# Performance work log

Measured on AMD Instinct MI355X. Metric: run time of the kernel, lower is better.

Reference implementation:

```python
import jax, jax.numpy as jnp
import numpy as np

C_IN, C_OUT, K, DG, PAD = 256, 256, 3, 2, 1
EPS = 1e-5


def setup_inputs() -> dict:
    key = jax.random.key(0)
    k = jax.random.split(key, 8)
    B, H, W = 4, 64, 64
    x = jax.random.normal(k[0], (B, C_IN, H, W), jnp.float32)
    # offset/mask conv (DCNv2 pack): 3 * dg * k * k output channels
    w_off = jax.random.normal(k[1], (3 * DG * K * K, C_IN, K, K), jnp.float32) * 0.01
    b_off = jnp.zeros((3 * DG * K * K,), jnp.float32)
    # main deformable conv weight
    w = jax.random.normal(k[2], (C_OUT, C_IN, K, K), jnp.float32) * (1.0 / np.sqrt(C_IN * K * K))
    b = jnp.zeros((C_OUT,), jnp.float32)
    # BatchNorm (eval mode: running stats)
    gamma = jnp.ones((C_OUT,), jnp.float32)
    beta = jnp.zeros((C_OUT,), jnp.float32)
    running_mean = jax.random.normal(k[3], (C_OUT,), jnp.float32) * 0.1
    running_var = jax.random.uniform(k[4], (C_OUT,), jnp.float32, 0.5, 1.5)
    return dict(x=x, w_off=w_off, b_off=b_off, w=w, b=b, gamma=gamma, beta=beta,
                running_mean=running_mean, running_var=running_var)


def _conv2d_same(x, w, b):
    y = jax.lax.conv_general_dilated(x, w, (1, 1), 'SAME',
                                     dimension_numbers=('NCHW', 'OIHW', 'NCHW'))
    return y + b[None, :, None, None]


def _deform_conv(x, w_off, b_off, w, b):
    B, C, H, W = x.shape
    K2 = K * K
    Cg = C // DG
    # offsets + modulation mask from internal conv (DCNv2 pack)
    om = _conv2d_same(x, w_off, b_off)            # [B, 3*DG*K2, H, W]
    o1, o2, m = jnp.split(om, 3, axis=1)
    mask = jax.nn.sigmoid(m).reshape(B, DG, 1, K2, H * W)
    off_y = o1.reshape(B, DG, K2, H, W)
    off_x = o2.reshape(B, DG, K2, H, W)
    # base sampling grid: output pixel + kernel tap - pad
    ki = jnp.arange(K)
    ky = (jnp.repeat(ki, K) - PAD).astype(jnp.float32)   # [K2]
    kx = (jnp.tile(ki, K) - PAD).astype(jnp.float32)     # [K2]
    py = off_y + ky[:, None, None] + jnp.arange(H, dtype=jnp.float32)[None, :, None]
    px = off_x + kx[:, None, None] + jnp.arange(W, dtype=jnp.float32)[None, None, :]
    y0 = jnp.floor(py)
    x0 = jnp.floor(px)
    ly = (py - y0).reshape(B, DG, 1, K2, H * W)
    lx = (px - x0).reshape(B, DG, 1, K2, H * W)
    y0i = y0.astype(jnp.int32)
    x0i = x0.astype(jnp.int32)
    xg = x.reshape(B, DG, Cg, H * W)

    def gather(yi, xi):
        # zero-padded bilinear corner gather, per deformable group
        valid = (yi >= 0) & (yi < H) & (xi >= 0) & (xi < W)
        lin = jnp.clip(yi, 0, H - 1) * W + jnp.clip(xi, 0, W - 1)
        v = jnp.take_along_axis(xg[:, :, :, None, :],
                                lin.reshape(B, DG, 1, K2, H * W), axis=-1)
        return v * valid.reshape(B, DG, 1, K2, H * W)

    val = (gather(y0i, x0i) * (1 - ly) * (1 - lx)
           + gather(y0i, x0i + 1) * (1 - ly) * lx
           + gather(y0i + 1, x0i) * ly * (1 - lx)
           + gather(y0i + 1, x0i + 1) * ly * lx)
    val = val * mask                               # [B, DG, Cg, K2, H*W]
    wr = w.reshape(C_OUT, DG, Cg, K2)
    out = jnp.einsum('bgckn,ogck->bon', val, wr).reshape(B, C_OUT, H, W)
    return out + b[None, :, None, None]


def reference(x, w_off, b_off, w, b, gamma, beta, running_mean, running_var):
    y = _deform_conv(x, w_off, b_off, w, b)
    inv = gamma / jnp.sqrt(running_var + EPS)
    y = (y - running_mean[None, :, None, None]) * inv[None, :, None, None] + beta[None, :, None, None]
    return jax.nn.relu(y)
```

## Files before the change

### kernel.cpp

```cpp
#include <hip/hip_runtime.h>
#include <math.h>

typedef __bf16 bf16x8 __attribute__((ext_vector_type(8)));
typedef float  f32x4  __attribute__((ext_vector_type(4)));
typedef int    i32x4  __attribute__((ext_vector_type(4)));

#define MFMA16(a, b, c) __builtin_amdgcn_mfma_f32_16x16x32_bf16((a), (b), (c), 0, 0, 0)

#define ATIDX(r, c) ((r) * 128 + (((c) ^ ((r) & 7)) * 8))

__global__ __launch_bounds__(256) void setup_kernel(
    const float* __restrict__ x, const float* __restrict__ w,
    const float* __restrict__ w_off, const float* __restrict__ bconv,
    const float* __restrict__ gamma, const float* __restrict__ beta,
    const float* __restrict__ mean, const float* __restrict__ var,
    __bf16* __restrict__ xT, __bf16* __restrict__ wFragD,
    __bf16* __restrict__ wFragO, float* __restrict__ sc,
    float* __restrict__ sh) {
  int t = threadIdx.x;
  if (blockIdx.x < 1024) {
    __shared__ float xs[64][65];
    int b = blockIdx.x >> 8, y = (blockIdx.x >> 2) & 63, cc = blockIdx.x & 3;
    for (int i = t; i < 4096; i += 256) {
      int cl = i >> 6, xc = i & 63;
      xs[cl][xc] = x[(((size_t)b * 256 + cc * 64 + cl) * 64 + y) * 64 + xc];
    }
    __syncthreads();
    for (int i = t; i < 4096; i += 256) {
      int xc = i >> 6, cl = i & 63;
      xT[(((size_t)b * 64 + y) * 64 + xc) * 256 + cc * 64 + cl] = (__bf16)xs[cl][xc];
    }
    return;
  }
  int i = (blockIdx.x - 1024) * 256 + t;
  if (i < 589824) {
    int j = i & 7, lane = (i >> 3) & 63, ocb = (i >> 9) & 15;
    int kc = (i >> 13) & 3, gk = i >> 15;
    int klocal = (lane >> 4) * 8 + j;
    int oc = ocb * 16 + (lane & 15);
    int c = kc * 32 + klocal;
    int g = gk / 9, ktap = gk % 9;
    wFragD[i] = (__bf16)w[((size_t)oc * 256 + g * 128 + c) * 9 + ktap];
  } else {
    int i2 = i - 589824;
    int j = i2 & 7, lane = (i2 >> 3) & 63, ocb = (i2 >> 9) & 3;
    int kc = (i2 >> 11) & 7, tap = i2 >> 14;
    int klocal = (lane >> 4) * 8 + j;
    int oc = ocb * 16 + (lane & 15);
    int ci = kc * 32 + klocal;
    wFragO[i2] = (oc < 54) ? (__bf16)w_off[((size_t)oc * 256 + ci) * 9 + tap]
                           : (__bf16)0.f;
  }
  if (i < 256) {
    float s = gamma[i] * rsqrtf(var[i] + 1e-5f);
    sc[i] = s;
    sh[i] = (bconv[i] - mean[i]) * s + beta[i];
  }
}

struct PhaseC {
  f32x4 swgtv[18 * 64];
  i32x4 slinv[18 * 64];
  __bf16 atile[2][64 * 128];
};
union FusedLDS {
  __bf16 rowbuf[3 * 66 * 256];
  PhaseC c;
};

__global__ __launch_bounds__(512) void fused_kernel(
    const __bf16* __restrict__ xT, const __bf16* __restrict__ wFragD,
    const __bf16* __restrict__ wFragO, const float* __restrict__ b_off,
    const float* __restrict__ sc, const float* __restrict__ sh,
    float* __restrict__ out) {
  __shared__ __attribute__((aligned(16))) FusedLDS U;
  __shared__ float omrow[54 * 64];
  int t = threadIdx.x;
  int b = blockIdx.x >> 6, y = blockIdx.x & 63;
  int lane = t & 63, wv = t >> 6;
  int l15 = lane & 15, quad = lane >> 4;
  const __bf16* xTb = xT + (size_t)b * 64 * 64 * 256;
  bf16x8 z8;
  #pragma unroll
  for (int e = 0; e < 8; ++e) z8[e] = (__bf16)0.f;

  for (int i = t; i < 3 * 66 * 32; i += 512) {
    int c = i & 31, px66 = (i >> 5) % 66, dy = i / 2112;
    int y2 = y + dy - 1, x2 = px66 - 1;
    bf16x8 v = z8;
    if (y2 >= 0 && y2 < 64 && x2 >= 0 && x2 < 64)
      v = *(const bf16x8*)(xTb + ((size_t)y2 * 64 + x2) * 256 + c * 8);
    *(bf16x8*)&U.rowbuf[dy * 16896 + px66 * 256 + ((c ^ (px66 & 7)) * 8)] = v;
  }
  __syncthreads();

  {
    int mh = wv & 1, ocq = wv >> 1;
    f32x4 acc0 = {0.f, 0.f, 0.f, 0.f};
    f32x4 acc1 = {0.f, 0.f, 0.f, 0.f};
    for (int tap = 0; tap < 9; ++tap) {
      int dy = tap / 3, dxs = tap % 3;
      const __bf16* bb = wFragO + ((size_t)(tap * 8) * 4 + ocq) * 512 + lane * 8;
      bf16x8 Bf[8];
      #pragma unroll
      for (int kc = 0; kc < 8; ++kc)
        Bf[kc] = *(const bf16x8*)(bb + (size_t)kc * 4 * 512);
      int p0 = mh * 32 + l15 + dxs, p1 = p0 + 16;
      const __bf16* rb = U.rowbuf + dy * 16896;
      #pragma unroll
      for (int kc = 0; kc < 8; ++kc) {
        int c = kc * 4 + quad;
        bf16x8 a0 = *(const bf16x8*)&rb[p0 * 256 + ((c ^ (p0 & 7)) * 8)];
        bf16x8 a1 = *(const bf16x8*)&rb[p1 * 256 + ((c ^ (p1 & 7)) * 8)];
        acc0 = MFMA16(a0, Bf[kc], acc0);
        acc1 = MFMA16(a1, Bf[kc], acc1);
      }
    }
    int oc = ocq * 16 + l15;
    if (oc < 54) {
      float bo = b_off[oc];
      #pragma unroll
      for (int fm = 0; fm < 2; ++fm) {
        f32x4 v = fm ? acc1 : acc0;
        f32x4 r = {v.x + bo, v.y + bo, v.z + bo, v.w + bo};
        int pxs = mh * 32 + fm * 16 + quad * 4;
        *(f32x4*)&omrow[oc * 64 + pxs] = r;
      }
    }
  }
  __syncthreads();

  for (int i = t; i < 18 * 64; i += 512) {
    int gk = i >> 6, p = i & 63;
    int k = gk % 9;
    float oy = omrow[gk * 64 + p];
    float ox = omrow[(18 + gk) * 64 + p];
    float mz = omrow[(36 + gk) * 64 + p];
    float mv = 1.f / (1.f + expf(-mz));
    float py  = (float)(y + (k / 3) - 1) + oy;
    float pxf = (float)(p + (k % 3) - 1) + ox;
    float y0f = floorf(py), x0f = floorf(pxf);
    int y0 = (int)y0f, x0 = (int)x0f;
    float ly = py - y0f, lx = pxf - x0f;
    int y1 = y0 + 1, x1 = x0 + 1;
    bool vy0 = (y0 >= 0) && (y0 < 64), vy1 = (y1 >= 0) && (y1 < 64);
    bool vx0 = (x0 >= 0) && (x0 < 64), vx1 = (x1 >= 0) && (x1 < 64);
    int cy0 = min(max(y0, 0), 63), cy1 = min(max(y1, 0), 63);
    int cx0 = min(max(x0, 0), 63), cx1 = min(max(x1, 0), 63);
    f32x4 sv;
    sv.x = (vy0 && vx0) ? (1.f - ly) * (1.f - lx) * mv : 0.f;
    sv.y = (vy0 && vx1) ? (1.f - ly) * lx * mv : 0.f;
    sv.z = (vy1 && vx0) ? ly * (1.f - lx) * mv : 0.f;
    sv.w = (vy1 && vx1) ? ly * lx * mv : 0.f;
    i32x4 lv;
    lv.x = (cy0 * 64 + cx0) * 256;
    lv.y = (cy0 * 64 + cx1) * 256;
    lv.z = (cy1 * 64 + cx0) * 256;
    lv.w = (cy1 * 64 + cx1) * 256;
    U.c.swgtv[i] = sv;
    U.c.slinv[i] = lv;
  }

  f32x4 acc[4][2];
  #pragma unroll
  for (int fm = 0; fm < 4; ++fm)
    #pragma unroll
    for (int fn = 0; fn < 2; ++fn)
      acc[fm][fn] = (f32x4){0.f, 0.f, 0.f, 0.f};

  __syncthreads();

  int ch0 = l15 * 8;
  {
    const __bf16* xg = xTb + ch0;
    #pragma unroll
    for (int j = 0; j < 2; ++j) {
      int p = wv * 8 + j * 4 + quad;
      f32x4 sv = U.c.swgtv[p];
      i32x4 lv = U.c.slinv[p];
      bf16x8 c0 = *(const bf16x8*)(xg + lv.x);
      bf16x8 c1 = *(const bf16x8*)(xg + lv.y);
      bf16x8 c2 = *(const bf16x8*)(xg + lv.z);
      bf16x8 c3 = *(const bf16x8*)(xg + lv.w);
      bf16x8 o;
      #pragma unroll
      for (int e = 0; e < 8; ++e)
        o[e] = (__bf16)(sv.x * (float)c0[e] + sv.y * (float)c1[e]
                      + sv.z * (float)c2[e] + sv.w * (float)c3[e]);
      *(bf16x8*)&U.c.atile[0][ATIDX(p, l15)] = o;
    }
  }
  bf16x8 Bf[8];
  {
    const __bf16* bb = wFragD + ((size_t)wv * 2) * 512 + lane * 8;
    #pragma unroll
    for (int kc = 0; kc < 4; ++kc) {
      Bf[kc * 2]     = *(const bf16x8*)(bb + (size_t)kc * 16 * 512);
      Bf[kc * 2 + 1] = *(const bf16x8*)(bb + (size_t)kc * 16 * 512 + 512);
    }
  }

  for (int gk = 0; gk < 18; ++gk) {
    __syncthreads();
    bf16x8 cr[2][4];
    f32x4 sv[2];
    int pj[2];
    if (gk < 17) {
      int gn = gk + 1;
      const __bf16* xg = xTb + (gn / 9) * 128 + ch0;
      #pragma unroll
      for (int j = 0; j < 2; ++j) {
        int p = wv * 8 + j * 4 + quad;
        pj[j] = p;
        sv[j] = U.c.swgtv[gn * 64 + p];
        i32x4 lv = U.c.slinv[gn * 64 + p];
        cr[j][0] = *(const bf16x8*)(xg + lv.x);
        cr[j][1] = *(const bf16x8*)(xg + lv.y);
        cr[j][2] = *(const bf16x8*)(xg + lv.z);
        cr[j][3] = *(const bf16x8*)(xg + lv.w);
      }
    }
    const __bf16* at = U.c.atile[gk & 1];
    #pragma unroll
    for (int kc = 0; kc < 4; ++kc) {
      #pragma unroll
      for (int fm = 0; fm < 4; ++fm) {
        bf16x8 a = *(const bf16x8*)&at[ATIDX(fm * 16 + l15, kc * 4 + quad)];
        acc[fm][0] = MFMA16(a, Bf[kc * 2],     acc[fm][0]);
        acc[fm][1] = MFMA16(a, Bf[kc * 2 + 1], acc[fm][1]);
      }
    }
    if (gk < 17) {
      __bf16* dst = U.c.atile[(gk + 1) & 1];
      #pragma unroll
      for (int j = 0; j < 2; ++j) {
        bf16x8 o;
        #pragma unroll
        for (int e = 0; e < 8; ++e)
          o[e] = (__bf16)(sv[j].x * (float)cr[j][0][e] + sv[j].y * (float)cr[j][1][e]
                        + sv[j].z * (float)cr[j][2][e] + sv[j].w * (float)cr[j][3][e]);
        *(bf16x8*)&dst[ATIDX(pj[j], l15)] = o;
      }
      const __bf16* bb = wFragD + ((size_t)((gk + 1) * 4) * 16 + wv * 2) * 512 + lane * 8;
      #pragma unroll
      for (int kc = 0; kc < 4; ++kc) {
        Bf[kc * 2]     = *(const bf16x8*)(bb + (size_t)kc * 16 * 512);
        Bf[kc * 2 + 1] = *(const bf16x8*)(bb + (size_t)kc * 16 * 512 + 512);
      }
    }
  }

  #pragma unroll
  for (int fm = 0; fm < 4; ++fm) {
    #pragma unroll
    for (int fn = 0; fn < 2; ++fn) {
      int oc = wv * 32 + fn * 16 + l15;
      float s = sc[oc], h = sh[oc];
      f32x4 v = acc[fm][fn];
      f32x4 r = {fmaxf(v.x * s + h, 0.f), fmaxf(v.y * s + h, 0.f),
                 fmaxf(v.z * s + h, 0.f), fmaxf(v.w * s + h, 0.f)};
      int pxs = fm * 16 + quad * 4;
      *(f32x4*)(out + (((size_t)b * 256 + oc) * 64 + y) * 64 + pxs) = r;
    }
  }
}

extern "C" void kernel_launch(void* const* d_in, const int* in_sizes, int n_in,
                              void* d_out, int out_size, void* d_ws, size_t ws_size,
                              hipStream_t stream) {
  const float* x     = (const float*)d_in[0];
  const float* w_off = (const float*)d_in[1];
  const float* b_off = (const float*)d_in[2];
  const float* w     = (const float*)d_in[3];
  const float* bconv = (const float*)d_in[4];
  const float* gamma = (const float*)d_in[5];
  const float* beta  = (const float*)d_in[6];
  const float* rmean = (const float*)d_in[7];
  const float* rvar  = (const float*)d_in[8];
  float* out = (float*)d_out;

  __bf16* xT     = (__bf16*)d_ws;
  __bf16* wFragD = (__bf16*)((char*)d_ws + 8388608);
  __bf16* wFragO = (__bf16*)((char*)d_ws + 9568256);
  float*  sc     = (float*)((char*)d_ws + 9863168);
  float*  sh     = (float*)((char*)d_ws + 9864192);

  setup_kernel<<<1024 + 2880, 256, 0, stream>>>(
      x, w, w_off, bconv, gamma, beta, rmean, rvar, xT, wFragD, wFragO, sc, sh);
  fused_kernel<<<4 * 64, 512, 0, stream>>>(xT, wFragD, wFragO, b_off, sc, sh, out);
}
```

Measured before the change: 131.5 us.

## Warp-specialize deformable conv into gather and MFMA waves, coalesce weight repack

The fused kernel now runs 1024 threads per block. Eight waves do the bilinear gather for the next tap group while the other eight run the MFMA GEMM on the current tile, replacing the old scheme where every wave did both in turn. The offset conv is split across 16 waves with one M tile each, and B fragments are streamed per k-chunk instead of held as eight registers. The setup kernel repacks the weights through shared memory in per-block tiles so global reads are coalesced, cutting the block count. The risk is that only half the waves issue MFMAs, and the larger block may hurt register allocation and occupancy.

```diff
diff --git a/kernel.cpp b/kernel.cpp
--- a/kernel.cpp
+++ b/kernel.cpp
@@ -17,44 +17,63 @@
     __bf16* __restrict__ xT, __bf16* __restrict__ wFragD,
     __bf16* __restrict__ wFragO, float* __restrict__ sc,
     float* __restrict__ sh) {
+  __shared__ float ws[16 * 128 * 9];
   int t = threadIdx.x;
   if (blockIdx.x < 1024) {
-    __shared__ float xs[64][65];
     int b = blockIdx.x >> 8, y = (blockIdx.x >> 2) & 63, cc = blockIdx.x & 3;
     for (int i = t; i < 4096; i += 256) {
       int cl = i >> 6, xc = i & 63;
-      xs[cl][xc] = x[(((size_t)b * 256 + cc * 64 + cl) * 64 + y) * 64 + xc];
+      ws[cl * 65 + xc] = x[(((size_t)b * 256 + cc * 64 + cl) * 64 + y) * 64 + xc];
     }
     __syncthreads();
     for (int i = t; i < 4096; i += 256) {
       int xc = i >> 6, cl = i & 63;
-      xT[(((size_t)b * 64 + y) * 64 + xc) * 256 + cc * 64 + cl] = (__bf16)xs[cl][xc];
+      xT[(((size_t)b * 64 + y) * 64 + xc) * 256 + cc * 64 + cl] =
+          (__bf16)ws[cl * 65 + xc];
     }
     return;
   }
-  int i = (blockIdx.x - 1024) * 256 + t;
-  if (i < 589824) {
-    int j = i & 7, lane = (i >> 3) & 63, ocb = (i >> 9) & 15;
-    int kc = (i >> 13) & 3, gk = i >> 15;
-    int klocal = (lane >> 4) * 8 + j;
-    int oc = ocb * 16 + (lane & 15);
-    int c = kc * 32 + klocal;
-    int g = gk / 9, ktap = gk % 9;
-    wFragD[i] = (__bf16)w[((size_t)oc * 256 + g * 128 + c) * 9 + ktap];
-  } else {
-    int i2 = i - 589824;
-    int j = i2 & 7, lane = (i2 >> 3) & 63, ocb = (i2 >> 9) & 3;
-    int kc = (i2 >> 11) & 7, tap = i2 >> 14;
-    int klocal = (lane >> 4) * 8 + j;
-    int oc = ocb * 16 + (lane & 15);
-    int ci = kc * 32 + klocal;
-    wFragO[i2] = (oc < 54) ? (__bf16)w_off[((size_t)oc * 256 + ci) * 9 + tap]
-                           : (__bf16)0.f;
-  }
-  if (i < 256) {
-    float s = gamma[i] * rsqrtf(var[i] + 1e-5f);
-    sc[i] = s;
-    sh[i] = (bconv[i] - mean[i]) * s + beta[i];
+  if (blockIdx.x < 1056) {
+    int id = blockIdx.x - 1024;
+    int g = id >> 4, ocb = id & 15;
+    for (int i = t; i < 18432; i += 256) {
+      int oc_l = i / 1152, rem = i % 1152;
+      ws[oc_l * 1152 + rem] = w[(size_t)(ocb * 16 + oc_l) * 2304 + g * 1152 + rem];
+    }
+    __syncthreads();
+    for (int i = t; i < 18432; i += 256) {
+      int j = i & 7, lane8 = (i >> 3) & 63, kc = (i >> 9) & 3, ktap = i >> 11;
+      int klocal = (lane8 >> 4) * 8 + j;
+      int oc_l = lane8 & 15, ci_l = kc * 32 + klocal;
+      float v = ws[oc_l * 1152 + ci_l * 9 + ktap];
+      int gk = g * 9 + ktap;
+      wFragD[((size_t)(gk * 4 + kc) * 16 + ocb) * 512 + (i & 511)] = (__bf16)v;
+    }
+    return;
+  }
+  {
+    int id2 = blockIdx.x - 1056;
+    int ocb = id2 >> 1, h = id2 & 1;
+    for (int i = t; i < 18432; i += 256) {
+      int oc_l = i / 1152, rem = i % 1152;
+      int oc = ocb * 16 + oc_l;
+      ws[oc_l * 1152 + rem] =
+          (oc < 54) ? w_off[(size_t)oc * 2304 + h * 1152 + rem] : 0.f;
+    }
+    __syncthreads();
+    for (int i = t; i < 18432; i += 256) {
+      int j = i & 7, lane8 = (i >> 3) & 63, kcl = (i >> 9) & 3, ktap = i >> 11;
+      int klocal = (lane8 >> 4) * 8 + j;
+      int oc_l = lane8 & 15, ci_l = kcl * 32 + klocal;
+      int kc = h * 4 + kcl;
+      float v = ws[oc_l * 1152 + ci_l * 9 + ktap];
+      wFragO[((size_t)(ktap * 8 + kc) * 4 + ocb) * 512 + (i & 511)] = (__bf16)v;
+    }
+    if (id2 == 0 && t < 256) {
+      float s = gamma[t] * rsqrtf(var[t] + 1e-5f);
+      sc[t] = s;
+      sh[t] = (bconv[t] - mean[t]) * s + beta[t];
+    }
   }
 }
 
@@ -68,7 +87,7 @@
   PhaseC c;
 };
 
-__global__ __launch_bounds__(512) void fused_kernel(
+__global__ __launch_bounds__(1024) void fused_kernel(
     const __bf16* __restrict__ xT, const __bf16* __restrict__ wFragD,
     const __bf16* __restrict__ wFragO, const float* __restrict__ b_off,
     const float* __restrict__ sc, const float* __restrict__ sh,
@@ -84,7 +103,7 @@
   #pragma unroll
   for (int e = 0; e < 8; ++e) z8[e] = (__bf16)0.f;
 
-  for (int i = t; i < 3 * 66 * 32; i += 512) {
+  for (int i = t; i < 3 * 66 * 32; i += 1024) {
     int c = i & 31, px66 = (i >> 5) % 66, dy = i / 2112;
     int y2 = y + dy - 1, x2 = px66 - 1;
     bf16x8 v = z8;
@@ -95,9 +114,8 @@
   __syncthreads();
 
   {
-    int mh = wv & 1, ocq = wv >> 1;
+    int mq = wv & 3, ocq = wv >> 2;
     f32x4 acc0 = {0.f, 0.f, 0.f, 0.f};
-    f32x4 acc1 = {0.f, 0.f, 0.f, 0.f};
     for (int tap = 0; tap < 9; ++tap) {
       int dy = tap / 3, dxs = tap % 3;
       const __bf16* bb = wFragO + ((size_t)(tap * 8) * 4 + ocq) * 512 + lane * 8;
@@ -105,32 +123,25 @@
       #pragma unroll
       for (int kc = 0; kc < 8; ++kc)
         Bf[kc] = *(const bf16x8*)(bb + (size_t)kc * 4 * 512);
-      int p0 = mh * 32 + l15 + dxs, p1 = p0 + 16;
+      int p0 = mq * 16 + l15 + dxs;
       const __bf16* rb = U.rowbuf + dy * 16896;
       #pragma unroll
       for (int kc = 0; kc < 8; ++kc) {
         int c = kc * 4 + quad;
         bf16x8 a0 = *(const bf16x8*)&rb[p0 * 256 + ((c ^ (p0 & 7)) * 8)];
-        bf16x8 a1 = *(const bf16x8*)&rb[p1 * 256 + ((c ^ (p1 & 7)) * 8)];
         acc0 = MFMA16(a0, Bf[kc], acc0);
-        acc1 = MFMA16(a1, Bf[kc], acc1);
       }
     }
     int oc = ocq * 16 + l15;
     if (oc < 54) {
       float bo = b_off[oc];
-      #pragma unroll
-      for (int fm = 0; fm < 2; ++fm) {
-        f32x4 v = fm ? acc1 : acc0;
-        f32x4 r = {v.x + bo, v.y + bo, v.z + bo, v.w + bo};
-        int pxs = mh * 32 + fm * 16 + quad * 4;
-        *(f32x4*)&omrow[oc * 64 + pxs] = r;
-      }
-    }
-  }
-  __syncthreads();
-
-  for (int i = t; i < 18 * 64; i += 512) {
+      f32x4 r = {acc0.x + bo, acc0.y + bo, acc0.z + bo, acc0.w + bo};
+      *(f32x4*)&omrow[oc * 64 + mq * 16 + quad * 4] = r;
+    }
+  }
+  __syncthreads();
+
+  for (int i = t; i < 18 * 64; i += 1024) {
     int gk = i >> 6, p = i & 63;
     int k = gk % 9;
     float oy = omrow[gk * 64 + p];
@@ -160,107 +171,99 @@
     U.c.swgtv[i] = sv;
     U.c.slinv[i] = lv;
   }
+  __syncthreads();
+
+  {
+    int p = t >> 4, c16 = t & 15;
+    const __bf16* xg = xTb + c16 * 8;
+    f32x4 sv = U.c.swgtv[p];
+    i32x4 lv = U.c.slinv[p];
+    bf16x8 c0 = *(const bf16x8*)(xg + lv.x);
+    bf16x8 c1 = *(const bf16x8*)(xg + lv.y);
+    bf16x8 c2 = *(const bf16x8*)(xg + lv.z);
+    bf16x8 c3 = *(const bf16x8*)(xg + lv.w);
+    bf16x8 o;
+    #pragma unroll
+    for (int e = 0; e < 8; ++e)
+      o[e] = (__bf16)(sv.x * (float)c0[e] + sv.y * (float)c1[e]
+                    + sv.z * (float)c2[e] + sv.w * (float)c3[e]);
+    *(bf16x8*)&U.c.atile[0][ATIDX(p, c16)] = o;
+  }
 
   f32x4 acc[4][2];
   #pragma unroll
-  for (int fm = 0; fm < 4; ++fm)
+  for (int fm = 0; fm < 4; ++fm) {
+    acc[fm][0] = (f32x4){0.f, 0.f, 0.f, 0.f};
+    acc[fm][1] = (f32x4){0.f, 0.f, 0.f, 0.f};
+  }
+  int nq = wv - 8;
+  bf16x8 bn0, bn1;
+  if (wv >= 8) {
+    const __bf16* bb = wFragD + ((size_t)nq * 2) * 512 + lane * 8;
+    bn0 = *(const bf16x8*)bb;
+    bn1 = *(const bf16x8*)(bb + 512);
+  }
+  __syncthreads();
+
+  for (int gk = 0; gk < 18; ++gk) {
+    if (wv < 8) {
+      if (gk < 17) {
+        int gn = gk + 1;
+        int c16 = t & 15, p = t >> 4;
+        const __bf16* xg = xTb + (gn / 9) * 128 + c16 * 8;
+        __bf16* dst = U.c.atile[(gk + 1) & 1];
+        #pragma unroll
+        for (int half = 0; half < 2; ++half) {
+          int pp = p + half * 32;
+          f32x4 sv = U.c.swgtv[gn * 64 + pp];
+          i32x4 lv = U.c.slinv[gn * 64 + pp];
+          bf16x8 c0 = *(const bf16x8*)(xg + lv.x);
+          bf16x8 c1 = *(const bf16x8*)(xg + lv.y);
+          bf16x8 c2 = *(const bf16x8*)(xg + lv.z);
+          bf16x8 c3 = *(const bf16x8*)(xg + lv.w);
+          bf16x8 o;
+          #pragma unroll
+          for (int e = 0; e < 8; ++e)
+            o[e] = (__bf16)(sv.x * (float)c0[e] + sv.y * (float)c1[e]
+                          + sv.z * (float)c2[e] + sv.w * (float)c3[e]);
+          *(bf16x8*)&dst[ATIDX(pp, c16)] = o;
+        }
+      }
+    } else {
+      const __bf16* at = U.c.atile[gk & 1];
+      #pragma unroll
+      for (int kc = 0; kc < 4; ++kc) {
+        bf16x8 b0 = bn0, b1 = bn1;
+        int nidx = gk * 4 + kc + 1;
+        if (nidx < 72) {
+          const __bf16* bb = wFragD + ((size_t)nidx * 16 + nq * 2) * 512 + lane * 8;
+          bn0 = *(const bf16x8*)bb;
+          bn1 = *(const bf16x8*)(bb + 512);
+        }
+        #pragma unroll
+        for (int fm = 0; fm < 4; ++fm) {
+          bf16x8 a = *(const bf16x8*)&at[ATIDX(fm * 16 + l15, kc * 4 + quad)];
+          acc[fm][0] = MFMA16(a, b0, acc[fm][0]);
+          acc[fm][1] = MFMA16(a, b1, acc[fm][1]);
+        }
+      }
+    }
+    __syncthreads();
+  }
+
+  if (wv >= 8) {
     #pragma unroll
-    for (int fn = 0; fn < 2; ++fn)
-      acc[fm][fn] = (f32x4){0.f, 0.f, 0.f, 0.f};
-
-  __syncthreads();
-
-  int ch0 = l15 * 8;
-  {
-    const __bf16* xg = xTb + ch0;
-    #pragma unroll
-    for (int j = 0; j < 2; ++j) {
-      int p = wv * 8 + j * 4 + quad;
-      f32x4 sv = U.c.swgtv[p];
-      i32x4 lv = U.c.slinv[p];
-      bf16x8 c0 = *(const bf16x8*)(xg + lv.x);
-      bf16x8 c1 = *(const bf16x8*)(xg + lv.y);
-      bf16x8 c2 = *(const bf16x8*)(xg + lv.z);
-      bf16x8 c3 = *(const bf16x8*)(xg + lv.w);
-      bf16x8 o;
-      #pragma unroll
-      for (int e = 0; e < 8; ++e)
-        o[e] = (__bf16)(sv.x * (float)c0[e] + sv.y * (float)c1[e]
-                      + sv.z * (float)c2[e] + sv.w * (float)c3[e]);
-      *(bf16x8*)&U.c.atile[0][ATIDX(p, l15)] = o;
-    }
-  }
-  bf16x8 Bf[8];
-  {
-    const __bf16* bb = wFragD + ((size_t)wv * 2) * 512 + lane * 8;
-    #pragma unroll
-    for (int kc = 0; kc < 4; ++kc) {
-      Bf[kc * 2]     = *(const bf16x8*)(bb + (size_t)kc * 16 * 512);
-      Bf[kc * 2 + 1] = *(const bf16x8*)(bb + (size_t)kc * 16 * 512 + 512);
-    }
-  }
-
-  for (int gk = 0; gk < 18; ++gk) {
-    __syncthreads();
-    bf16x8 cr[2][4];
-    f32x4 sv[2];
-    int pj[2];
-    if (gk < 17) {
-      int gn = gk + 1;
-      const __bf16* xg = xTb + (gn / 9) * 128 + ch0;
-      #pragma unroll
-      for (int j = 0; j < 2; ++j) {
-        int p = wv * 8 + j * 4 + quad;
-        pj[j] = p;
-        sv[j] = U.c.swgtv[gn * 64 + p];
-        i32x4 lv = U.c.slinv[gn * 64 + p];
-        cr[j][0] = *(const bf16x8*)(xg + lv.x);
-        cr[j][1] = *(const bf16x8*)(xg + lv.y);
-        cr[j][2] = *(const bf16x8*)(xg + lv.z);
-        cr[j][3] = *(const bf16x8*)(xg + lv.w);
-      }
-    }
-    const __bf16* at = U.c.atile[gk & 1];
-    #pragma unroll
-    for (int kc = 0; kc < 4; ++kc) {
-      #pragma unroll
-      for (int fm = 0; fm < 4; ++fm) {
-        bf16x8 a = *(const bf16x8*)&at[ATIDX(fm * 16 + l15, kc * 4 + quad)];
-        acc[fm][0] = MFMA16(a, Bf[kc * 2],     acc[fm][0]);
-        acc[fm][1] = MFMA16(a, Bf[kc * 2 + 1], acc[fm][1]);
-      }
-    }
-    if (gk < 17) {
-      __bf16* dst = U.c.atile[(gk + 1) & 1];
-      #pragma unroll
-      for (int j = 0; j < 2; ++j) {
-        bf16x8 o;
-        #pragma unroll
-        for (int e = 0; e < 8; ++e)
-          o[e] = (__bf16)(sv[j].x * (float)cr[j][0][e] + sv[j].y * (float)cr[j][1][e]
-                        + sv[j].z * (float)cr[j][2][e] + sv[j].w * (float)cr[j][3][e]);
-        *(bf16x8*)&dst[ATIDX(pj[j], l15)] = o;
-      }
-      const __bf16* bb = wFragD + ((size_t)((gk + 1) * 4) * 16 + wv * 2) * 512 + lane * 8;
-      #pragma unroll
-      for (int kc = 0; kc < 4; ++kc) {
-        Bf[kc * 2]     = *(const bf16x8*)(bb + (size_t)kc * 16 * 512);
-        Bf[kc * 2 + 1] = *(const bf16x8*)(bb + (size_t)kc * 16 * 512 + 512);
-      }
-    }
-  }
-
-  #pragma unroll
-  for (int fm = 0; fm < 4; ++fm) {
-    #pragma unroll
-    for (int fn = 0; fn < 2; ++fn) {
-      int oc = wv * 32 + fn * 16 + l15;
-      float s = sc[oc], h = sh[oc];
-      f32x4 v = acc[fm][fn];
-      f32x4 r = {fmaxf(v.x * s + h, 0.f), fmaxf(v.y * s + h, 0.f),
-                 fmaxf(v.z * s + h, 0.f), fmaxf(v.w * s + h, 0.f)};
-      int pxs = fm * 16 + quad * 4;
-      *(f32x4*)(out + (((size_t)b * 256 + oc) * 64 + y) * 64 + pxs) = r;
+    for (int fm = 0; fm < 4; ++fm) {
+      #pragma unroll
+      for (int fn = 0; fn < 2; ++fn) {
+        int oc = nq * 32 + fn * 16 + l15;
+        float s = sc[oc], h = sh[oc];
+        f32x4 v = acc[fm][fn];
+        f32x4 r = {fmaxf(v.x * s + h, 0.f), fmaxf(v.y * s + h, 0.f),
+                   fmaxf(v.z * s + h, 0.f), fmaxf(v.w * s + h, 0.f)};
+        int pxs = fm * 16 + quad * 4;
+        *(f32x4*)(out + (((size_t)b * 256 + oc) * 64 + y) * 64 + pxs) = r;
+      }
     }
   }
 }
@@ -285,7 +288,7 @@
   float*  sc     = (float*)((char*)d_ws + 9863168);
   float*  sh     = (float*)((char*)d_ws + 9864192);
 
-  setup_kernel<<<1024 + 2880, 256, 0, stream>>>(
+  setup_kernel<<<1064, 256, 0, stream>>>(
       x, w, w_off, bconv, gamma, beta, rmean, rvar, xT, wFragD, wFragO, sc, sh);
-  fused_kernel<<<4 * 64, 512, 0, stream>>>(xT, wFragD, wFragO, b_off, sc, sh, out);
+  fused_kernel<<<4 * 64, 1024, 0, stream>>>(xT, wFragD, wFragO, b_off, sc, sh, out);
 }
```

New measurement: 156.2 us. 1.19x slower.
